# Kernel optimization log

Measured on AMD Instinct MI355X. Metric: run time of the kernel, lower is better.

The kernel has to match this reference:

```python
import jax, jax.numpy as jnp
import numpy as np

N, E, F, H, L = 100000, 800000, 128, 128, 64


def _glorot(key, shape):
    lim = float(np.sqrt(6.0 / (shape[0] + shape[1])))
    return jax.random.uniform(key, shape, jnp.float32, -lim, lim)


def setup_inputs() -> dict:
    key = jax.random.key(0)
    ks = jax.random.split(key, 10)
    x = jax.random.normal(ks[0], (N, F), jnp.float32)
    noise = jax.random.normal(ks[1], (N, F), jnp.float32)
    edge_index = jax.random.randint(ks[2], (2, E), 0, N, jnp.int32)
    return {
        "x": x,
        "noise": noise,
        "edge_index": edge_index,
        "bn_gamma": jnp.ones((F,), jnp.float32),
        "bn_beta": jnp.zeros((F,), jnp.float32),
        "W1": _glorot(ks[3], (F, H)),
        "b1": jnp.zeros((H,), jnp.float32),
        "W2": _glorot(ks[4], (H + 2 * F, H)),
        "b2": jnp.zeros((H,), jnp.float32),
        "Wm": _glorot(ks[5], (H + F, L)),
        "bm": jnp.zeros((L,), jnp.float32),
        "Ws": _glorot(ks[6], (H + F, L)),
        "bs": jnp.zeros((L,), jnp.float32),
    }


def _gcn_conv(x, W, b, src, dst, norm, n):
    # GCNConv: transform, then sym-normalized sparse aggregation, then bias
    h = x @ W                                 # [n, out]
    msg = h[src] * norm[:, None]              # gather + scale  [E', out]
    return jax.ops.segment_sum(msg, dst, num_segments=n) + b


def reference(x, noise, edge_index, bn_gamma, bn_beta, W1, b1, W2, b2, Wm, bm, Ws, bs):
    n = x.shape[0]
    loops = jnp.arange(n, dtype=edge_index.dtype)
    src = jnp.concatenate([edge_index[0], loops])  # add self-loops
    dst = jnp.concatenate([edge_index[1], loops])
    deg = jax.ops.segment_sum(jnp.ones_like(src, dtype=x.dtype), dst, num_segments=n)
    dinv = jnp.where(deg > 0, jax.lax.rsqrt(jnp.maximum(deg, 1e-12)), 0.0)
    norm = dinv[src] * dinv[dst]                   # D^-1/2 A D^-1/2 edge weights

    # bn1 (training-mode batch norm over nodes)
    mu = x.mean(axis=0)
    var = x.var(axis=0)
    xb = (x - mu) * jax.lax.rsqrt(var + 1e-5) * bn_gamma + bn_beta

    h1 = jax.nn.relu(_gcn_conv(xb, W1, b1, src, dst, norm, n))
    h1 = jnp.concatenate([xb, noise, h1], axis=1)  # [n, H + 2F]
    h2 = jax.nn.relu(_gcn_conv(h1, W2, b2, src, dst, norm, n))
    # dropout(p=0.4) in eval mode -> identity
    last = jnp.concatenate([xb, h2], axis=1)       # [n, F + H]
    z_mean = _gcn_conv(last, Wm, bm, src, dst, norm, n)
    z_logstd = _gcn_conv(last, Ws, bs, src, dst, norm, n)
    return (z_mean, z_logstd)
```

## Files before the change

kernel.cpp:

```cpp
#include <hip/hip_runtime.h>
#include <math.h>


typedef short bf16x8 __attribute__((ext_vector_type(8)));
typedef float f32x4 __attribute__((ext_vector_type(4)));
typedef float f32x2 __attribute__((ext_vector_type(2)));

#define BN_G 1024
#define SCAN_BLK 256
#define SCAN_ELEMS 1024

__device__ inline unsigned short f2bf(float f) {
    unsigned int u = __builtin_bit_cast(unsigned int, f);
    u += 0x7fff + ((u >> 16) & 1);
    return (unsigned short)(u >> 16);
}
__device__ inline unsigned int pack2(float lo, float hi) {
    return ((unsigned int)f2bf(hi) << 16) | f2bf(lo);
}
__device__ inline f32x2 unp(unsigned int u) {
    return (f32x2){__builtin_bit_cast(float, u << 16),
                   __builtin_bit_cast(float, u & 0xffff0000u)};
}
__device__ inline void acc8v(f32x2* a, uint4 v) {
    a[0] += unp(v.x); a[1] += unp(v.y); a[2] += unp(v.z); a[3] += unp(v.w);
}
__device__ inline ushort4 cvt4(float4 v) {
    ushort4 o;
    o.x = f2bf(v.x); o.y = f2bf(v.y); o.z = f2bf(v.z); o.w = f2bf(v.w);
    return o;
}

__device__ __forceinline__ void gload_lds16(const void* g, void* l) {
    __builtin_amdgcn_global_load_lds(
        (const __attribute__((address_space(1))) unsigned int*)g,
        (__attribute__((address_space(3))) unsigned int*)l, 16, 0, 0);
}

__global__ __launch_bounds__(256) void fused1(const float4* __restrict__ x4,
                                              float* __restrict__ partials, int n,
                                              ushort4* __restrict__ x16,
                                              const int* __restrict__ ei,
                                              int* __restrict__ cnt,
                                              int* __restrict__ slot, int E) {
    __shared__ float4 lds[2][8][32];
    int bid = blockIdx.x, t = threadIdx.x;
    if (bid < BN_G) {
        int cg = t & 31;
        int rs = t >> 5;
        float4 s = make_float4(0.f, 0.f, 0.f, 0.f);
        float4 q = make_float4(0.f, 0.f, 0.f, 0.f);
        const float4 z4 = make_float4(0.f, 0.f, 0.f, 0.f);
        const int stride = BN_G * 32;
        for (int r0 = bid * 32 + rs * 4; r0 < n; r0 += stride) {
            float4 v0 = x4[(size_t)r0 * 32 + cg];
            float4 v1 = (r0 + 1 < n) ? x4[(size_t)(r0 + 1) * 32 + cg] : z4;
            float4 v2 = (r0 + 2 < n) ? x4[(size_t)(r0 + 2) * 32 + cg] : z4;
            float4 v3 = (r0 + 3 < n) ? x4[(size_t)(r0 + 3) * 32 + cg] : z4;
            x16[(size_t)r0 * 32 + cg] = cvt4(v0);
            if (r0 + 1 < n) x16[(size_t)(r0 + 1) * 32 + cg] = cvt4(v1);
            if (r0 + 2 < n) x16[(size_t)(r0 + 2) * 32 + cg] = cvt4(v2);
            if (r0 + 3 < n) x16[(size_t)(r0 + 3) * 32 + cg] = cvt4(v3);
            s.x += v0.x + v1.x + v2.x + v3.x;
            s.y += v0.y + v1.y + v2.y + v3.y;
            s.z += v0.z + v1.z + v2.z + v3.z;
            s.w += v0.w + v1.w + v2.w + v3.w;
            q.x = fmaf(v0.x, v0.x, fmaf(v1.x, v1.x, fmaf(v2.x, v2.x, fmaf(v3.x, v3.x, q.x))));
            q.y = fmaf(v0.y, v0.y, fmaf(v1.y, v1.y, fmaf(v2.y, v2.y, fmaf(v3.y, v3.y, q.y))));
            q.z = fmaf(v0.z, v0.z, fmaf(v1.z, v1.z, fmaf(v2.z, v2.z, fmaf(v3.z, v3.z, q.z))));
            q.w = fmaf(v0.w, v0.w, fmaf(v1.w, v1.w, fmaf(v2.w, v2.w, fmaf(v3.w, v3.w, q.w))));
        }
        lds[0][rs][cg] = s;
        lds[1][rs][cg] = q;
        __syncthreads();
        if (t < 64) {
            int which = t >> 5;
            int c = t & 31;
            float4 a = lds[which][0][c];
#pragma unroll
            for (int i = 1; i < 8; i++) {
                float4 b = lds[which][i][c];
                a.x += b.x; a.y += b.y; a.z += b.z; a.w += b.w;
            }
            int base = which * 128 + c * 4;
            partials[(size_t)(base + 0) * BN_G + bid] = a.x;
            partials[(size_t)(base + 1) * BN_G + bid] = a.y;
            partials[(size_t)(base + 2) * BN_G + bid] = a.z;
            partials[(size_t)(base + 3) * BN_G + bid] = a.w;
        }
        return;
    }
    int e = (bid - BN_G) * 256 + t;
    if (e < E) slot[e] = atomicAdd(&cnt[ei[E + e]], 1);
}

__global__ __launch_bounds__(256) void fused2(const float4* __restrict__ partials4,
                                              float* __restrict__ stats,
                                              const int* __restrict__ cnt,
                                              int* __restrict__ row_ptr,
                                              int* __restrict__ bsums, int n) {
    __shared__ float red[256];
    __shared__ int lds[SCAN_BLK];
    int t = threadIdx.x;
    if (blockIdx.x < 256) {
        int c = blockIdx.x;
        float4 v = partials4[(size_t)c * (BN_G / 4) + t];
        red[t] = v.x + v.y + v.z + v.w;
        __syncthreads();
        for (int off = 128; off > 0; off >>= 1) {
            if (t < off) red[t] += red[t + off];
            __syncthreads();
        }
        if (t == 0) stats[c] = red[0];
    } else {
        int blk = blockIdx.x - 256;
        int base = blk * SCAN_ELEMS;
        int v[4];
        int s = 0;
#pragma unroll
        for (int j = 0; j < 4; j++) {
            int i = base + t * 4 + j;
            v[j] = s;
            s += (i < n) ? cnt[i] : 0;
        }
        lds[t] = s;
        __syncthreads();
        for (int off = 1; off < SCAN_BLK; off <<= 1) {
            int val = (t >= off) ? lds[t - off] : 0;
            __syncthreads();
            lds[t] += val;
            __syncthreads();
        }
        int excl = (t == 0) ? 0 : lds[t - 1];
#pragma unroll
        for (int j = 0; j < 4; j++) {
            int i = base + t * 4 + j;
            if (i < n) row_ptr[i] = excl + v[j];
        }
        if (t == SCAN_BLK - 1) bsums[blk] = lds[t];
    }
}

__global__ void fused3(int* __restrict__ bsums, int nb,
                       const float* __restrict__ stats,
                       const float* __restrict__ gamma, const float* __restrict__ beta,
                       float* __restrict__ scale, float* __restrict__ shift, float invN) {
    int t = threadIdx.x;
    if (t == 0) {
        int acc = 0;
        for (int i = 0; i < nb; i++) { int c = bsums[i]; bsums[i] = acc; acc += c; }
    } else if (t >= 128 && t < 256) {
        int c = t - 128;
        float mu = stats[c] * invN;
        float var = stats[128 + c] * invN - mu * mu;
        float sc = gamma[c] / sqrtf(var + 1e-5f);
        scale[c] = sc;
        shift[c] = beta[c] - mu * sc;
    }
}

__global__ void fused4(int* __restrict__ row_ptr, const int* __restrict__ bsums,
                       const int* __restrict__ cnt, float* __restrict__ dinv,
                       int n, int E) {
    int i = blockIdx.x * blockDim.x + threadIdx.x;
    if (i < n) {
        row_ptr[i] += bsums[i / SCAN_ELEMS];
        dinv[i] = rsqrtf((float)cnt[i] + 1.0f);
    }
    if (i == 0) row_ptr[n] = E;
}

__device__ inline void pack_body(int i, const float* __restrict__ W,
                                 unsigned short* __restrict__ Wp,
                                 int K, int C, int colOff,
                                 const float* __restrict__ scale) {
    if (i >= K * C) return;
    int k = i / C, c = i % C;
    float v = W[i];
    if (k < 128) v *= scale[k];
    int gc = c + colOff;
    int s = k >> 7, kc = (k >> 5) & 3, lhi = (k >> 3) & 3, j = k & 7;
    int wc = gc >> 6, n = (gc >> 4) & 3, l15 = gc & 15;
    int lane = lhi * 16 + l15;
    size_t dst = ((size_t)((s * 2 + wc) * 4 + kc) * 4 + n) * 512 + lane * 8 + j;
    Wp[dst] = f2bf(v);
}

__global__ __launch_bounds__(256) void fused5(
    const int* __restrict__ ei, const int* __restrict__ row_ptr,
    const int* __restrict__ slot, int* __restrict__ edge_src, int E, int EB,
    const float4* __restrict__ n4, ushort4* __restrict__ nb4, int total4, int CB,
    const float* __restrict__ scale, const float* __restrict__ shift,
    const float* __restrict__ W1, unsigned short* __restrict__ Wp1,
    const float* __restrict__ W2, unsigned short* __restrict__ Wp2,
    const float* __restrict__ Wm, const float* __restrict__ Ws,
    unsigned short* __restrict__ Wpc,
    float* __restrict__ cv1, float* __restrict__ cv2, float* __restrict__ cvc)
{
    __shared__ float cred[256];
    int bid = blockIdx.x, t = threadIdx.x;
    if (bid < EB) {
        int e = bid * 256 + t;
        if (e < E) {
            int s = ei[e], d = ei[E + e];
            edge_src[row_ptr[d] + slot[e]] = s;
        }
        return;
    }
    bid -= EB;
    if (bid < CB) {
        int i = bid * 256 + t;
        if (i < total4) nb4[i] = cvt4(n4[i]);
        return;
    }
    bid -= CB;
    if (bid < 64)  { pack_body(bid * 256 + t, W1, Wp1, 128, 128, 0, scale); return; }
    bid -= 64;
    if (bid < 192) { pack_body(bid * 256 + t, W2, Wp2, 384, 128, 0, scale); return; }
    bid -= 192;
    if (bid < 64)  { pack_body(bid * 256 + t, Wm, Wpc, 256, 64, 0, scale); return; }
    bid -= 64;
    if (bid < 64)  { pack_body(bid * 256 + t, Ws, Wpc, 256, 64, 64, scale); return; }
    bid -= 64;
    {
        int c = t & 127, kh = t >> 7;
        float s = 0.f;
        if (bid == 0) {
            for (int k = kh * 64; k < kh * 64 + 64; k++)
                s = fmaf(shift[k], W1[k * 128 + c], s);
        } else if (bid == 1) {
            for (int k = kh * 64; k < kh * 64 + 64; k++)
                s = fmaf(shift[k], W2[k * 128 + c], s);
        } else {
            const float* Wsrc = (c < 64) ? Wm : Ws;
            int cc = (c < 64) ? c : c - 64;
            for (int k = kh * 64; k < kh * 64 + 64; k++)
                s = fmaf(shift[k], Wsrc[k * 64 + cc], s);
        }
        cred[t] = s;
        __syncthreads();
        if (t < 128) {
            float v = cred[t] + cred[t + 128];
            float* dst = (bid == 0) ? cv1 : (bid == 1) ? cv2 : cvc;
            dst[c] = v;
        }
    }
}

template <int NSRC>
__global__ __launch_bounds__(256, 4) void gemm_mfma(
    const unsigned short* __restrict__ A0, const unsigned short* __restrict__ A1,
    const unsigned short* __restrict__ A2,
    const unsigned short* __restrict__ Wpk,
    const float* __restrict__ dinv, const float* __restrict__ cvec,
    unsigned short* __restrict__ out)
{
    constexpr int NBUF = (NSRC > 1) ? 2 : 1;
    __shared__ unsigned char ldsA[NBUF][64 * 256];

    const int lane = threadIdx.x & 63;
    const int wid  = threadIdx.x >> 6;
    const int wr   = wid >> 1, wc = wid & 1;
    const int l15  = lane & 15, lhi = lane >> 4;
    const int c0   = wc * 64;
    const long rowblk = (long)blockIdx.x * 64;
    const int rl0 = wr * 32 + l15;
    const int rl1 = rl0 + 16;
    const int rsw = rl0 & 7;

    const unsigned short* __restrict__ srcs[3] = {A0, A1, A2};
    auto stage = [&](int s, int b) {
#pragma unroll
        for (int i = 0; i < 4; i++) {
            int G = (wid * 4 + i) * 64 + lane;
            int r = G >> 4, g = G & 15;
            const unsigned short* src = srcs[s] + (rowblk + r) * 128 + (g ^ (r & 7)) * 8;
            gload_lds16(src, &ldsA[b][G * 16]);
        }
    };

    f32x4 acc[2][4];
#pragma unroll
    for (int g = 0; g < 2; g++)
#pragma unroll
        for (int n = 0; n < 4; n++)
            acc[g][n] = (f32x4){0.f, 0.f, 0.f, 0.f};

    stage(0, 0);

#pragma unroll
    for (int s = 0; s < NSRC; s++) {
        const unsigned short* wbase = Wpk + ((size_t)(s * 2 + wc) * 16) * 512 + lane * 8;
        bf16x8 w[4][4];
#pragma unroll
        for (int kc = 0; kc < 4; kc++)
#pragma unroll
            for (int n = 0; n < 4; n++)
                w[kc][n] = *reinterpret_cast<const bf16x8*>(wbase + (kc * 4 + n) * 512);

        __syncthreads();
        if (s + 1 < NSRC) stage(s + 1, (s + 1) % NBUF);
        const unsigned char* bufp = ldsA[s % NBUF];

#pragma unroll
        for (int kc = 0; kc < 4; kc++) {
            int g0 = kc * 4 + lhi;
            bf16x8 a0 = *reinterpret_cast<const bf16x8*>(bufp + rl0 * 256 + (g0 ^ rsw) * 16);
            bf16x8 a1 = *reinterpret_cast<const bf16x8*>(bufp + rl1 * 256 + (g0 ^ rsw) * 16);
#pragma unroll
            for (int n = 0; n < 4; n++) {
                acc[0][n] = __builtin_amdgcn_mfma_f32_16x16x32_bf16(w[kc][n], a0, acc[0][n], 0, 0, 0);
                acc[1][n] = __builtin_amdgcn_mfma_f32_16x16x32_bf16(w[kc][n], a1, acc[1][n], 0, 0, 0);
            }
        }
    }

    float4 cv[4];
#pragma unroll
    for (int n = 0; n < 4; n++)
        cv[n] = *reinterpret_cast<const float4*>(cvec + c0 + n * 16 + lhi * 4);

#pragma unroll
    for (int g = 0; g < 2; g++) {
        long row = rowblk + (g ? rl1 : rl0);
        float dv = dinv[row];
        unsigned short* op = out + row * 128 + c0 + lhi * 4;
#pragma unroll
        for (int n = 0; n < 4; n++) {
            f32x4 v = acc[g][n];
            ushort4 pk;
            pk.x = f2bf((v[0] + cv[n].x) * dv);
            pk.y = f2bf((v[1] + cv[n].y) * dv);
            pk.z = f2bf((v[2] + cv[n].z) * dv);
            pk.w = f2bf((v[3] + cv[n].w) * dv);
            *reinterpret_cast<ushort4*>(op + n * 16) = pk;
        }
    }
}

template <bool RELU>
__global__ void gather16(const uint4* __restrict__ hs4, const float* __restrict__ dinv,
                         const int* __restrict__ row_ptr, const int* __restrict__ edge_src,
                         const float* __restrict__ bias, uint4* __restrict__ out4, int n) {
    int node = blockIdx.x * 16 + (threadIdx.x >> 4);
    if (node >= n) return;
    int cl = threadIdx.x & 15;
    int beg = row_ptr[node], end = row_ptr[node + 1];
    f32x2 a[4] = {(f32x2){0.f,0.f}, (f32x2){0.f,0.f}, (f32x2){0.f,0.f}, (f32x2){0.f,0.f}};
    f32x2 b[4] = {(f32x2){0.f,0.f}, (f32x2){0.f,0.f}, (f32x2){0.f,0.f}, (f32x2){0.f,0.f}};
    acc8v(a, hs4[(size_t)node * 16 + cl]);
    int e = beg;
    for (; e + 4 <= end; e += 4) {
        uint4 v0 = hs4[(size_t)edge_src[e] * 16 + cl];
        uint4 v1 = hs4[(size_t)edge_src[e + 1] * 16 + cl];
        uint4 v2 = hs4[(size_t)edge_src[e + 2] * 16 + cl];
        uint4 v3 = hs4[(size_t)edge_src[e + 3] * 16 + cl];
        acc8v(a, v0);
        acc8v(b, v1);
        acc8v(a, v2);
        acc8v(b, v3);
    }
    if (e + 2 <= end) {
        uint4 v0 = hs4[(size_t)edge_src[e] * 16 + cl];
        uint4 v1 = hs4[(size_t)edge_src[e + 1] * 16 + cl];
        acc8v(a, v0);
        acc8v(b, v1);
        e += 2;
    }
    if (e < end) acc8v(a, hs4[(size_t)edge_src[e] * 16 + cl]);
#pragma unroll
    for (int i = 0; i < 4; i++) a[i] += b[i];
    float dv = dinv[node];
    float4 b0 = *reinterpret_cast<const float4*>(bias + cl * 8);
    float4 b1 = *reinterpret_cast<const float4*>(bias + cl * 8 + 4);
    float r0 = fmaf(a[0].x, dv, b0.x), r1 = fmaf(a[0].y, dv, b0.y);
    float r2 = fmaf(a[1].x, dv, b0.z), r3 = fmaf(a[1].y, dv, b0.w);
    float r4 = fmaf(a[2].x, dv, b1.x), r5 = fmaf(a[2].y, dv, b1.y);
    float r6 = fmaf(a[3].x, dv, b1.z), r7 = fmaf(a[3].y, dv, b1.w);
    if (RELU) {
        r0 = fmaxf(r0, 0.f); r1 = fmaxf(r1, 0.f); r2 = fmaxf(r2, 0.f); r3 = fmaxf(r3, 0.f);
        r4 = fmaxf(r4, 0.f); r5 = fmaxf(r5, 0.f); r6 = fmaxf(r6, 0.f); r7 = fmaxf(r7, 0.f);
    }
    uint4 o;
    o.x = pack2(r0, r1); o.y = pack2(r2, r3);
    o.z = pack2(r4, r5); o.w = pack2(r6, r7);
    out4[(size_t)node * 16 + cl] = o;
}

__global__ void gather_dual(const uint4* __restrict__ hs4, const float* __restrict__ dinv,
                            const int* __restrict__ row_ptr, const int* __restrict__ edge_src,
                            const float* __restrict__ bm, const float* __restrict__ bs,
                            float* __restrict__ zm, float* __restrict__ zs, int n) {
    int node = blockIdx.x * 16 + (threadIdx.x >> 4);
    if (node >= n) return;
    int cl = threadIdx.x & 15;
    int beg = row_ptr[node], end = row_ptr[node + 1];
    f32x2 a[4] = {(f32x2){0.f,0.f}, (f32x2){0.f,0.f}, (f32x2){0.f,0.f}, (f32x2){0.f,0.f}};
    f32x2 b[4] = {(f32x2){0.f,0.f}, (f32x2){0.f,0.f}, (f32x2){0.f,0.f}, (f32x2){0.f,0.f}};
    acc8v(a, hs4[(size_t)node * 16 + cl]);
    int e = beg;
    for (; e + 4 <= end; e += 4) {
        uint4 v0 = hs4[(size_t)edge_src[e] * 16 + cl];
        uint4 v1 = hs4[(size_t)edge_src[e + 1] * 16 + cl];
        uint4 v2 = hs4[(size_t)edge_src[e + 2] * 16 + cl];
        uint4 v3 = hs4[(size_t)edge_src[e + 3] * 16 + cl];
        acc8v(a, v0);
        acc8v(b, v1);
        acc8v(a, v2);
        acc8v(b, v3);
    }
    if (e + 2 <= end) {
        uint4 v0 = hs4[(size_t)edge_src[e] * 16 + cl];
        uint4 v1 = hs4[(size_t)edge_src[e + 1] * 16 + cl];
        acc8v(a, v0);
        acc8v(b, v1);
        e += 2;
    }
    if (e < end) acc8v(a, hs4[(size_t)edge_src[e] * 16 + cl]);
#pragma unroll
    for (int i = 0; i < 4; i++) a[i] += b[i];
    float dv = dinv[node];
    const float* bp = (cl < 8) ? (bm + cl * 8) : (bs + (cl - 8) * 8);
    float* zp = (cl < 8) ? (zm + (size_t)node * 64 + cl * 8)
                         : (zs + (size_t)node * 64 + (cl - 8) * 8);
    float4 b0 = *reinterpret_cast<const float4*>(bp);
    float4 b1 = *reinterpret_cast<const float4*>(bp + 4);
    float4 o0 = make_float4(fmaf(a[0].x, dv, b0.x), fmaf(a[0].y, dv, b0.y),
                            fmaf(a[1].x, dv, b0.z), fmaf(a[1].y, dv, b0.w));
    float4 o1 = make_float4(fmaf(a[2].x, dv, b1.x), fmaf(a[2].y, dv, b1.y),
                            fmaf(a[3].x, dv, b1.z), fmaf(a[3].y, dv, b1.w));
    *reinterpret_cast<float4*>(zp) = o0;
    *reinterpret_cast<float4*>(zp + 4) = o1;
}


extern "C" void kernel_launch(void* const* d_in, const int* in_sizes, int n_in,
                              void* d_out, int out_size, void* d_ws, size_t ws_size,
                              hipStream_t stream) {
    const float* x     = (const float*)d_in[0];
    const float* noise = (const float*)d_in[1];
    const int*   ei    = (const int*)d_in[2];
    const float* gamma = (const float*)d_in[3];
    const float* beta  = (const float*)d_in[4];
    const float* W1    = (const float*)d_in[5];
    const float* b1    = (const float*)d_in[6];
    const float* W2    = (const float*)d_in[7];
    const float* b2    = (const float*)d_in[8];
    const float* Wm    = (const float*)d_in[9];
    const float* bm    = (const float*)d_in[10];
    const float* Ws    = (const float*)d_in[11];
    const float* bs    = (const float*)d_in[12];

    const int N  = in_sizes[0] / 128;
    const int E  = in_sizes[2] / 2;
    const int NPAD = (N + 127) & ~127;
    const int nb = (N + SCAN_ELEMS - 1) / SCAN_ELEMS;
    const int EB = (E + 255) / 256;
    const int CB = (N * 32 + 255) / 256;

    auto align256 = [](size_t b) { return (b + 255) & ~(size_t)255; };
    char* p = (char*)d_ws;
    int* cnt      = (int*)p;  p += align256((size_t)N * 4);
    int* row_ptr  = (int*)p;  p += align256((size_t)(N + 1) * 4);
    int* edge_src = (int*)p;  p += align256((size_t)E * 4);
    int* slot     = (int*)p;  p += align256((size_t)E * 4);
    int* bsums    = (int*)p;  p += align256((size_t)nb * 4);
    float* dinv   = (float*)p; p += align256((size_t)NPAD * 4);
    float* stats  = (float*)p; p += align256(512 * 4);
    float* cv1    = (float*)p; p += align256(128 * 4);
    float* cv2    = (float*)p; p += align256(128 * 4);
    float* cvc    = (float*)p; p += align256(128 * 4);
    float* bnpart = (float*)p; p += align256((size_t)256 * BN_G * 4);
    unsigned short* Wp1 = (unsigned short*)p; p += align256(128 * 128 * 2);
    unsigned short* Wp2 = (unsigned short*)p; p += align256(128 * 384 * 2);
    unsigned short* Wpc = (unsigned short*)p; p += align256(128 * 256 * 2);
    unsigned short* x16 = (unsigned short*)p; p += align256((size_t)NPAD * 128 * 2);
    unsigned short* n16 = (unsigned short*)p; p += align256((size_t)NPAD * 128 * 2);
    unsigned short* h16 = (unsigned short*)p; p += align256((size_t)NPAD * 128 * 2);

    float* scale = stats + 256;
    float* shift = stats + 384;

    float* dout = (float*)d_out;
    unsigned short* hs12 = (unsigned short*)d_out;
    unsigned short* hs3  = n16;
    float* zm = dout;
    float* zs = dout + (size_t)N * 64;

    const int gblocks = NPAD / 64;
    const int nblocks16 = (N + 15) / 16;

    hipMemsetAsync(cnt, 0, (size_t)N * 4, stream);
    fused1<<<BN_G + EB, 256, 0, stream>>>((const float4*)x, bnpart, N,
                                          (ushort4*)x16, ei, cnt, slot, E);
    fused2<<<256 + nb, 256, 0, stream>>>((const float4*)bnpart, stats, cnt, row_ptr, bsums, N);
    fused3<<<1, 256, 0, stream>>>(bsums, nb, stats, gamma, beta, scale, shift, 1.0f / (float)N);
    fused4<<<(N + 255) / 256, 256, 0, stream>>>(row_ptr, bsums, cnt, dinv, N, E);
    fused5<<<EB + CB + 384 + 3, 256, 0, stream>>>(
        ei, row_ptr, slot, edge_src, E, EB,
        (const float4*)noise, (ushort4*)n16, N * 32, CB,
        scale, shift, W1, Wp1, W2, Wp2, Wm, Ws, Wpc, cv1, cv2, cvc);

    gemm_mfma<1><<<gblocks, 256, 0, stream>>>(x16, nullptr, nullptr, Wp1, dinv, cv1, hs12);
    gather16<true><<<nblocks16, 256, 0, stream>>>((const uint4*)hs12, dinv, row_ptr,
                                                  edge_src, b1, (uint4*)h16, N);
    gemm_mfma<3><<<gblocks, 256, 0, stream>>>(x16, n16, h16, Wp2, dinv, cv2, hs12);
    gather16<true><<<nblocks16, 256, 0, stream>>>((const uint4*)hs12, dinv, row_ptr,
                                                  edge_src, b2, (uint4*)h16, N);
    gemm_mfma<2><<<gblocks, 256, 0, stream>>>(x16, h16, nullptr, Wpc, dinv, cvc, hs3);
    gather_dual<<<nblocks16, 256, 0, stream>>>((const uint4*)hs3, dinv, row_ptr,
                                               edge_src, bm, bs, zm, zs, N);
}
```

Baseline: 272.6 us.

## Fold preprocessing kernels via last-block ticket and merge first GEMM into scatter kernel

Removes the single-block fused3 kernel by having the last block of fused2, found through an atomic ticket, do the block-sum scan and the batch-norm scale/shift. The row_ptr fixup and dinv computation now run in the same kernel as the weight packing. The first GEMM (x16 @ Wp1) is merged into the edge-scatter and noise-conversion kernel, so independent work shares one launch and one fewer launch boundary. This cuts launch count and idle tail time, at the cost of an extra memset, threadfence and atomic overhead, and a larger heterogeneous kernel with LDS use on every block.

```diff
diff --git a/kernel.cpp b/kernel.cpp
--- a/kernel.cpp
+++ b/kernel.cpp
@@ -98,9 +98,15 @@
                                               float* __restrict__ stats,
                                               const int* __restrict__ cnt,
                                               int* __restrict__ row_ptr,
-                                              int* __restrict__ bsums, int n) {
+                                              int* __restrict__ bsums, int n, int nb,
+                                              int* __restrict__ ticket,
+                                              const float* __restrict__ gamma,
+                                              const float* __restrict__ beta,
+                                              float* __restrict__ scale,
+                                              float* __restrict__ shift, float invN) {
     __shared__ float red[256];
     __shared__ int lds[SCAN_BLK];
+    __shared__ int amLast;
     int t = threadIdx.x;
     if (blockIdx.x < 256) {
         int c = blockIdx.x;
@@ -139,35 +145,25 @@
         }
         if (t == SCAN_BLK - 1) bsums[blk] = lds[t];
     }
-}
-
-__global__ void fused3(int* __restrict__ bsums, int nb,
-                       const float* __restrict__ stats,
-                       const float* __restrict__ gamma, const float* __restrict__ beta,
-                       float* __restrict__ scale, float* __restrict__ shift, float invN) {
-    int t = threadIdx.x;
-    if (t == 0) {
-        int acc = 0;
-        for (int i = 0; i < nb; i++) { int c = bsums[i]; bsums[i] = acc; acc += c; }
-    } else if (t >= 128 && t < 256) {
-        int c = t - 128;
-        float mu = stats[c] * invN;
-        float var = stats[128 + c] * invN - mu * mu;
-        float sc = gamma[c] / sqrtf(var + 1e-5f);
-        scale[c] = sc;
-        shift[c] = beta[c] - mu * sc;
-    }
-}
-
-__global__ void fused4(int* __restrict__ row_ptr, const int* __restrict__ bsums,
-                       const int* __restrict__ cnt, float* __restrict__ dinv,
-                       int n, int E) {
-    int i = blockIdx.x * blockDim.x + threadIdx.x;
-    if (i < n) {
-        row_ptr[i] += bsums[i / SCAN_ELEMS];
-        dinv[i] = rsqrtf((float)cnt[i] + 1.0f);
-    }
-    if (i == 0) row_ptr[n] = E;
+    __threadfence();
+    __syncthreads();
+    if (t == 0) amLast = (atomicAdd(ticket, 1) == 256 + nb - 1);
+    __syncthreads();
+    if (amLast) {
+        __threadfence();
+        if (t == 0) {
+            int acc = 0;
+            for (int i = 0; i < nb; i++) { int c = bsums[i]; bsums[i] = acc; acc += c; }
+        }
+        if (t >= 128 && t < 256) {
+            int c = t - 128;
+            float mu = stats[c] * invN;
+            float var = stats[128 + c] * invN - mu * mu;
+            float sc = gamma[c] / sqrtf(var + 1e-5f);
+            scale[c] = sc;
+            shift[c] = beta[c] - mu * sc;
+        }
+    }
 }
 
 __device__ inline void pack_body(int i, const float* __restrict__ W,
@@ -186,10 +182,9 @@
     Wp[dst] = f2bf(v);
 }
 
-__global__ __launch_bounds__(256) void fused5(
-    const int* __restrict__ ei, const int* __restrict__ row_ptr,
-    const int* __restrict__ slot, int* __restrict__ edge_src, int E, int EB,
-    const float4* __restrict__ n4, ushort4* __restrict__ nb4, int total4, int CB,
+__global__ __launch_bounds__(256) void fused4(
+    int* __restrict__ row_ptr, const int* __restrict__ bsums,
+    const int* __restrict__ cnt, float* __restrict__ dinv, int n, int E, int NB,
     const float* __restrict__ scale, const float* __restrict__ shift,
     const float* __restrict__ W1, unsigned short* __restrict__ Wp1,
     const float* __restrict__ W2, unsigned short* __restrict__ Wp2,
@@ -199,21 +194,16 @@
 {
     __shared__ float cred[256];
     int bid = blockIdx.x, t = threadIdx.x;
-    if (bid < EB) {
-        int e = bid * 256 + t;
-        if (e < E) {
-            int s = ei[e], d = ei[E + e];
-            edge_src[row_ptr[d] + slot[e]] = s;
-        }
+    if (bid < NB) {
+        int i = bid * 256 + t;
+        if (i < n) {
+            row_ptr[i] += bsums[i / SCAN_ELEMS];
+            dinv[i] = rsqrtf((float)cnt[i] + 1.0f);
+        }
+        if (i == 0) row_ptr[n] = E;
         return;
     }
-    bid -= EB;
-    if (bid < CB) {
-        int i = bid * 256 + t;
-        if (i < total4) nb4[i] = cvt4(n4[i]);
-        return;
-    }
-    bid -= CB;
+    bid -= NB;
     if (bid < 64)  { pack_body(bid * 256 + t, W1, Wp1, 128, 128, 0, scale); return; }
     bid -= 64;
     if (bid < 192) { pack_body(bid * 256 + t, W2, Wp2, 384, 128, 0, scale); return; }
@@ -247,6 +237,100 @@
     }
 }
 
+__global__ __launch_bounds__(256, 4) void fused5(
+    const int* __restrict__ ei, const int* __restrict__ row_ptr,
+    const int* __restrict__ slot, int* __restrict__ edge_src, int E, int EB,
+    const unsigned short* __restrict__ x16, const unsigned short* __restrict__ Wp1,
+    const float* __restrict__ dinv, const float* __restrict__ cv1,
+    unsigned short* __restrict__ hs_out, int GB,
+    const float4* __restrict__ n4, ushort4* __restrict__ nb4, int total4)
+{
+    __shared__ unsigned char ldsA[64 * 256];
+    int bid = blockIdx.x, t = threadIdx.x;
+    if (bid < EB) {
+        int e = bid * 256 + t;
+        if (e < E) {
+            int s = ei[e], d = ei[E + e];
+            edge_src[row_ptr[d] + slot[e]] = s;
+        }
+        return;
+    }
+    bid -= EB;
+    if (bid < GB) {
+        const int lane = t & 63;
+        const int wid  = t >> 6;
+        const int wr   = wid >> 1, wc = wid & 1;
+        const int l15  = lane & 15, lhi = lane >> 4;
+        const int c0   = wc * 64;
+        const long rowblk = (long)bid * 64;
+        const int rl0 = wr * 32 + l15;
+        const int rl1 = rl0 + 16;
+        const int rsw = rl0 & 7;
+
+#pragma unroll
+        for (int i = 0; i < 4; i++) {
+            int G = (wid * 4 + i) * 64 + lane;
+            int r = G >> 4, g = G & 15;
+            gload_lds16(x16 + (rowblk + r) * 128 + (g ^ (r & 7)) * 8, &ldsA[G * 16]);
+        }
+
+        f32x4 acc[2][4];
+#pragma unroll
+        for (int g = 0; g < 2; g++)
+#pragma unroll
+            for (int n = 0; n < 4; n++)
+                acc[g][n] = (f32x4){0.f, 0.f, 0.f, 0.f};
+
+        const unsigned short* wbase = Wp1 + ((size_t)wc * 16) * 512 + lane * 8;
+        bf16x8 w[4][4];
+#pragma unroll
+        for (int kc = 0; kc < 4; kc++)
+#pragma unroll
+            for (int n = 0; n < 4; n++)
+                w[kc][n] = *reinterpret_cast<const bf16x8*>(wbase + (kc * 4 + n) * 512);
+
+        __syncthreads();
+
+#pragma unroll
+        for (int kc = 0; kc < 4; kc++) {
+            int g0 = kc * 4 + lhi;
+            bf16x8 a0 = *reinterpret_cast<const bf16x8*>(ldsA + rl0 * 256 + (g0 ^ rsw) * 16);
+            bf16x8 a1 = *reinterpret_cast<const bf16x8*>(ldsA + rl1 * 256 + (g0 ^ rsw) * 16);
+#pragma unroll
+            for (int n = 0; n < 4; n++) {
+                acc[0][n] = __builtin_amdgcn_mfma_f32_16x16x32_bf16(w[kc][n], a0, acc[0][n], 0, 0, 0);
+                acc[1][n] = __builtin_amdgcn_mfma_f32_16x16x32_bf16(w[kc][n], a1, acc[1][n], 0, 0, 0);
+            }
+        }
+
+        float4 cv[4];
+#pragma unroll
+        for (int n = 0; n < 4; n++)
+            cv[n] = *reinterpret_cast<const float4*>(cv1 + c0 + n * 16 + lhi * 4);
+
+#pragma unroll
+        for (int g = 0; g < 2; g++) {
+            long row = rowblk + (g ? rl1 : rl0);
+            float dv = dinv[row];
+            unsigned short* op = hs_out + row * 128 + c0 + lhi * 4;
+#pragma unroll
+            for (int n = 0; n < 4; n++) {
+                f32x4 v = acc[g][n];
+                ushort4 pk;
+                pk.x = f2bf((v[0] + cv[n].x) * dv);
+                pk.y = f2bf((v[1] + cv[n].y) * dv);
+                pk.z = f2bf((v[2] + cv[n].z) * dv);
+                pk.w = f2bf((v[3] + cv[n].w) * dv);
+                *reinterpret_cast<ushort4*>(op + n * 16) = pk;
+            }
+        }
+        return;
+    }
+    bid -= GB;
+    int i = bid * 256 + t;
+    if (i < total4) nb4[i] = cvt4(n4[i]);
+}
+
 template <int NSRC>
 __global__ __launch_bounds__(256, 4) void gemm_mfma(
     const unsigned short* __restrict__ A0, const unsigned short* __restrict__ A1,
@@ -457,10 +541,12 @@
     const int nb = (N + SCAN_ELEMS - 1) / SCAN_ELEMS;
     const int EB = (E + 255) / 256;
     const int CB = (N * 32 + 255) / 256;
+    const int NB = (N + 255) / 256;
 
     auto align256 = [](size_t b) { return (b + 255) & ~(size_t)255; };
     char* p = (char*)d_ws;
     int* cnt      = (int*)p;  p += align256((size_t)N * 4);
+    int* ticket   = (int*)p;  p += 256;
     int* row_ptr  = (int*)p;  p += align256((size_t)(N + 1) * 4);
     int* edge_src = (int*)p;  p += align256((size_t)E * 4);
     int* slot     = (int*)p;  p += align256((size_t)E * 4);
@@ -491,17 +577,20 @@
     const int nblocks16 = (N + 15) / 16;
 
     hipMemsetAsync(cnt, 0, (size_t)N * 4, stream);
+    hipMemsetAsync(ticket, 0, 4, stream);
     fused1<<<BN_G + EB, 256, 0, stream>>>((const float4*)x, bnpart, N,
                                           (ushort4*)x16, ei, cnt, slot, E);
-    fused2<<<256 + nb, 256, 0, stream>>>((const float4*)bnpart, stats, cnt, row_ptr, bsums, N);
-    fused3<<<1, 256, 0, stream>>>(bsums, nb, stats, gamma, beta, scale, shift, 1.0f / (float)N);
-    fused4<<<(N + 255) / 256, 256, 0, stream>>>(row_ptr, bsums, cnt, dinv, N, E);
-    fused5<<<EB + CB + 384 + 3, 256, 0, stream>>>(
+    fused2<<<256 + nb, 256, 0, stream>>>((const float4*)bnpart, stats, cnt, row_ptr,
+                                         bsums, N, nb, ticket, gamma, beta,
+                                         scale, shift, 1.0f / (float)N);
+    fused4<<<NB + 384 + 3, 256, 0, stream>>>(row_ptr, bsums, cnt, dinv, N, E, NB,
+                                             scale, shift, W1, Wp1, W2, Wp2,
+                                             Wm, Ws, Wpc, cv1, cv2, cvc);
+    fused5<<<EB + gblocks + CB, 256, 0, stream>>>(
         ei, row_ptr, slot, edge_src, E, EB,
-        (const float4*)noise, (ushort4*)n16, N * 32, CB,
-        scale, shift, W1, Wp1, W2, Wp2, Wm, Ws, Wpc, cv1, cv2, cvc);
-
-    gemm_mfma<1><<<gblocks, 256, 0, stream>>>(x16, nullptr, nullptr, Wp1, dinv, cv1, hs12);
+        x16, Wp1, dinv, cv1, hs12, gblocks,
+        (const float4*)noise, (ushort4*)n16, N * 32);
+
     gather16<true><<<nblocks16, 256, 0, stream>>>((const uint4*)hs12, dinv, row_ptr,
                                                   edge_src, b1, (uint4*)h16, N);
     gemm_mfma<3><<<gblocks, 256, 0, stream>>>(x16, n16, h16, Wp2, dinv, cv2, hs12);
```

Measured after the change: 295.3 us. +8.3%, slower.
